# Kernel tuning notes

Hardware: AMD Instinct MI355X
Metric: run time of the kernel (lower is better)

The kernel has to match this reference:

```python
import jax, jax.numpy as jnp
import numpy as np

N_NODES = 100000
N_EDGES = 1600000
N_GRAPHS = 1024
B = 1024
GNN_INP, GNN_HID, GNN_OUT = 64, 128, 64
INP, HID, OUT = 64, 256, 1
EPS = 1e-5  # torch BatchNorm1d default eps


def _bn(h, gamma, beta):
    # training-mode BatchNorm1d: biased batch statistics over dim 0
    m = h.mean(axis=0)
    v = jnp.mean((h - m) ** 2, axis=0)
    return (h - m) * jax.lax.rsqrt(v + EPS) * gamma + beta


def setup_inputs() -> dict:
    key = jax.random.key(0)
    ks = jax.random.split(key, 24)
    s = 0.05
    inp = {
        "x": jax.random.normal(ks[0], (B, INP), jnp.float32),
        "masks": jax.random.randint(ks[1], (B,), 0, N_GRAPHS),
        "gnn_x": jax.random.normal(ks[2], (N_NODES, GNN_INP), jnp.float32),
        "edge_index": jax.random.randint(ks[3], (2, N_EDGES), 0, N_NODES),
        "gnn_batch": jnp.sort(jax.random.randint(ks[4], (N_NODES,), 0, N_GRAPHS)),
        # GCNConv params
        "W_gcn": jax.random.normal(ks[5], (GNN_INP, GNN_HID), jnp.float32) * s,
        "b_gcn": jnp.zeros((GNN_HID,), jnp.float32),
        "g1": jnp.ones((GNN_HID,), jnp.float32), "be1": jnp.zeros((GNN_HID,), jnp.float32),
        "W_lin1": jax.random.normal(ks[6], (GNN_HID, GNN_HID // 2), jnp.float32) * s,
        "b_lin1": jnp.zeros((GNN_HID // 2,), jnp.float32),
        "g2": jnp.ones((GNN_HID // 2,), jnp.float32), "be2": jnp.zeros((GNN_HID // 2,), jnp.float32),
        "W_lin2": jax.random.normal(ks[7], (GNN_HID // 2, GNN_OUT), jnp.float32) * s,
        "b_lin2": jnp.zeros((GNN_OUT,), jnp.float32),
        "g3": jnp.ones((GNN_OUT,), jnp.float32), "be3": jnp.zeros((GNN_OUT,), jnp.float32),
        # head params
        "W_fc1": jax.random.normal(ks[8], (INP + GNN_OUT, HID), jnp.float32) * s,
        "b_fc1": jnp.zeros((HID,), jnp.float32),
        "g4": jnp.ones((HID,), jnp.float32), "be4": jnp.zeros((HID,), jnp.float32),
        "W_fc2": jax.random.normal(ks[9], (HID, HID // 4), jnp.float32) * s,
        "b_fc2": jnp.zeros((HID // 4,), jnp.float32),
        "g5": jnp.ones((HID // 4,), jnp.float32), "be5": jnp.zeros((HID // 4,), jnp.float32),
        "W_fc3": jax.random.normal(ks[10], (HID // 4, OUT), jnp.float32) * s,
        "b_fc3": jnp.zeros((OUT,), jnp.float32),
    }
    return inp


def _forward(x, masks, gnn_x, edge_index, gnn_batch,
             W_gcn, b_gcn, g1, be1, W_lin1, b_lin1, g2, be2, W_lin2, b_lin2,
             g3, be3, W_fc1, b_fc1, g4, be4, W_fc2, b_fc2, g5, be5, W_fc3, b_fc3):
    N = gnn_x.shape[0]
    # --- GCNConv: linear transform, self-loops, sym-normalized scatter-add ---
    h = gnn_x @ W_gcn  # [N, GNN_HID]
    loop = jnp.arange(N)
    src = jnp.concatenate([edge_index[0], loop])
    dst = jnp.concatenate([edge_index[1], loop])
    deg = jax.ops.segment_sum(jnp.ones_like(dst, jnp.float32), dst, num_segments=N)
    dis = jax.lax.rsqrt(deg)  # deg >= 1 thanks to self-loops
    norm = dis[src] * dis[dst]  # [E+N]
    agg = jax.ops.segment_sum(h[src] * norm[:, None], dst, num_segments=N) + b_gcn
    z = jax.nn.relu(_bn(agg, g1, be1))  # dropout = identity (eval)
    # --- global_mean_pool over graph ids ---
    sums = jax.ops.segment_sum(z, gnn_batch, num_segments=N_GRAPHS)
    cnt = jax.ops.segment_sum(jnp.ones((N,), jnp.float32), gnn_batch, num_segments=N_GRAPHS)
    pooled = sums / jnp.maximum(cnt, 1.0)[:, None]  # [G, GNN_HID]
    z = jax.nn.relu(_bn(pooled @ W_lin1 + b_lin1, g2, be2))
    z = _bn(z @ W_lin2 + b_lin2, g3, be3)  # [G, GNN_OUT]
    # --- MixGNN head ---
    g = z[masks]  # [B, GNN_OUT]
    t = jnp.concatenate([x, g], axis=1)
    t = jax.nn.relu(_bn(t @ W_fc1 + b_fc1, g4, be4))
    t = t * t  # Multiply([h, h])
    t = jax.nn.relu(_bn(t @ W_fc2 + b_fc2, g5, be5))
    t = t * t
    t = t * t
    return t @ W_fc3 + b_fc3  # [B, OUT]


def reference(x, masks, gnn_x, edge_index, gnn_batch,
              W_gcn, b_gcn, g1, be1, W_lin1, b_lin1, g2, be2, W_lin2, b_lin2,
              g3, be3, W_fc1, b_fc1, g4, be4, W_fc2, b_fc2, g5, be5, W_fc3, b_fc3):
    return _forward(x, masks, gnn_x, edge_index, gnn_batch,
                    W_gcn, b_gcn, g1, be1, W_lin1, b_lin1, g2, be2, W_lin2, b_lin2,
                    g3, be3, W_fc1, b_fc1, g4, be4, W_fc2, b_fc2, g5, be5, W_fc3, b_fc3)
```

## Files before the change

kernel.cpp:

```cpp
#include <hip/hip_runtime.h>
#include <hip/hip_bf16.h>

#define N_NODES 100000
#define N_EDGES 1600000
#define N_GRAPHS 1024
#define BSZ 1024
#define EPS 1e-5f

#define NBUCK 256
#define BUCKW 391
#define BCAP  8192
#define SRC_MASK 0x1FFFF
#define BIN_CHUNK 4096
#define BIN_BLOCKS 391
#define NCHUNK 512
#define CHUNK_ROWS 196
#define CVT_BLOCKS 6250

#define WS_PSUM    0
#define WS_STATS1  131072
#define WS_STATS2  131200
#define WS_STATS4  131328
#define WS_STATS5  131840
#define WS_M       131968
#define WS_CS      136064
#define WS_ZTOTAL  136128
#define WS_GCUR    136128
#define WS_SCALE1  136384
#define WS_SHIFTP  136512
#define WS_GSTART  136640
#define WS_DIS     137668
#define WS_ROWPTR  237668
#define WS_ROWLEN  337668
#define WS_PACKED  437668
#define WS_CSRC    2534820
#define WS_XH      4631972
#define WS_AGGX    7831972
#define WS_T1      14231972
#define WS_T2      14297508
#define WS_T4      14363044
#define WS_T5      14625188

__device__ inline unsigned short f2bf(float f) {
    unsigned int u = __float_as_uint(f);
    return (unsigned short)((u + 0x7FFFu + ((u >> 16) & 1u)) >> 16);
}

__global__ __launch_bounds__(256) void prep_cvt_kernel(float* __restrict__ ws,
                                                       const int* __restrict__ gbatch,
                                                       const float* __restrict__ x,
                                                       unsigned short* __restrict__ xh) {
    int b = blockIdx.x, tid = threadIdx.x;
    if (b < CVT_BLOCKS) {
        int i = b * 256 + tid;
        float4 f = ((const float4*)x)[i];
        ushort4 h;
        h.x = f2bf(f.x); h.y = f2bf(f.y); h.z = f2bf(f.z); h.w = f2bf(f.w);
        ((ushort4*)xh)[i] = h;
    } else if (b < CVT_BLOCKS + 16) {
        for (int i = (b - CVT_BLOCKS) * 256 + tid; i < WS_ZTOTAL; i += 16 * 256) ws[i] = 0.0f;
    } else if (b == CVT_BLOCKS + 16) {
        ((int*)(ws + WS_GCUR))[tid] = tid * BCAP;
    } else {
        int g = (b - (CVT_BLOCKS + 17)) * 256 + tid;
        int lo = 0, hi = N_NODES;
        while (lo < hi) {
            int mid = (lo + hi) >> 1;
            if (gbatch[mid] < g) lo = mid + 1; else hi = mid;
        }
        int* gstart = (int*)(ws + WS_GSTART);
        gstart[g] = lo;
        if (g == 0) gstart[N_GRAPHS] = N_NODES;
    }
}

__global__ __launch_bounds__(512) void bin_kernel(const int* __restrict__ ei,
                                                  int* __restrict__ gcursor,
                                                  unsigned int* __restrict__ packed) {
    __shared__ unsigned int stage[BIN_CHUNK];
    __shared__ int lh[NBUCK], lbase[NBUCK], lcur[NBUCK], gb[NBUCK];
    const int* src = ei;
    const int* dst = ei + N_EDGES;
    int tid = threadIdx.x;
    int base = blockIdx.x * BIN_CHUNK;
    int n = min(BIN_CHUNK, N_EDGES - base);
    if (tid < NBUCK) lh[tid] = 0;
    __syncthreads();
    for (int i = tid; i < n; i += 512)
        atomicAdd(&lh[dst[base + i] / BUCKW], 1);
    __syncthreads();
    if (tid < NBUCK) lbase[tid] = lh[tid];
    __syncthreads();
    for (int off = 1; off < NBUCK; off <<= 1) {
        int t = (tid < NBUCK && tid >= off) ? lbase[tid - off] : 0;
        __syncthreads();
        if (tid < NBUCK) lbase[tid] += t;
        __syncthreads();
    }
    if (tid < NBUCK) {
        int excl = lbase[tid] - lh[tid];
        lbase[tid] = excl;
        lcur[tid] = excl;
        gb[tid] = atomicAdd(&gcursor[tid], lh[tid]);
    }
    __syncthreads();
    for (int i = tid; i < n; i += 512) {
        int d = dst[base + i];
        int s = src[base + i];
        int bk = d / BUCKW;
        int dl = d - bk * BUCKW;
        int slot = atomicAdd(&lcur[bk], 1);
        stage[slot] = ((unsigned int)dl << 17) | (unsigned int)s;
    }
    __syncthreads();
    int wid = tid >> 6, lane = tid & 63;
    for (int bk = wid; bk < NBUCK; bk += 8) {
        int lo = lbase[bk], go = gb[bk];
        int len = min(lh[bk], (bk + 1) * BCAP - go);
        for (int j = lane; j < len; j += 64)
            packed[go + j] = stage[lo + j];
    }
}

__global__ __launch_bounds__(512) void csr_build_kernel(const unsigned int* __restrict__ packed,
                                                        const int* __restrict__ gcur,
                                                        int* __restrict__ rowptr,
                                                        int* __restrict__ rowlen,
                                                        int* __restrict__ csrc,
                                                        float* __restrict__ dis) {
    __shared__ int dcnt[BUCKW];
    __shared__ int lcur[BUCKW];
    __shared__ int stage[BCAP];
    int b = blockIdx.x, tid = threadIdx.x;
    int e0 = b * BCAP;
    int ecnt = min(gcur[b] - e0, BCAP);
    int nbase = b * BUCKW;
    int nmax = min(BUCKW, N_NODES - nbase);
    for (int i = tid; i < BUCKW; i += 512) dcnt[i] = 0;
    __syncthreads();
    for (int i = tid; i < ecnt; i += 512)
        atomicAdd(&dcnt[packed[e0 + i] >> 17], 1);
    __syncthreads();
    for (int i = tid; i < nmax; i += 512) {
        dis[nbase + i] = rsqrtf((float)dcnt[i] + 1.0f);
        rowlen[nbase + i] = dcnt[i];
    }
    __syncthreads();
    if (tid < 64) {
        int lane = tid;
        int run = 0;
        for (int c = 0; c < BUCKW; c += 64) {
            int idx = c + lane;
            int v = (idx < BUCKW) ? dcnt[idx] : 0;
            int inc = v;
#pragma unroll
            for (int off = 1; off < 64; off <<= 1) {
                int t = __shfl_up(inc, off);
                if (lane >= off) inc += t;
            }
            if (idx < BUCKW) {
                int excl = run + inc - v;
                dcnt[idx] = excl;
                lcur[idx] = excl;
            }
            run += __shfl(inc, 63);
        }
    }
    __syncthreads();
    for (int i = tid; i < nmax; i += 512)
        rowptr[nbase + i] = e0 + dcnt[i];
    for (int i = tid; i < ecnt; i += 512) {
        unsigned int r = packed[e0 + i];
        int slot = atomicAdd(&lcur[r >> 17], 1);
        stage[slot] = (int)(r & SRC_MASK);
    }
    __syncthreads();
    for (int i = tid; i < ecnt; i += 512) csrc[e0 + i] = stage[i];
}

__global__ __launch_bounds__(256) void gather_kernel(const unsigned short* __restrict__ xh,
                                                     const int* __restrict__ rowptr,
                                                     const int* __restrict__ rowlen,
                                                     const int* __restrict__ csrc,
                                                     const float* __restrict__ dis,
                                                     float* __restrict__ aggx) {
    int wid = (blockIdx.x * 256 + threadIdx.x) >> 6;
    int lane = threadIdx.x & 63;
    if (wid >= N_NODES) return;
    int start = rowptr[wid];
    int len = rowlen[wid];
    float dd = dis[wid];
    float self = __uint_as_float((unsigned int)xh[(size_t)wid * 64 + lane] << 16);
    float acc = self * dd * dd;
    for (int j0 = 0; j0 < len; j0 += 64) {
        int cnt = min(64, len - j0);
        int sv = 0;
        float wv = 0.f;
        if (lane < cnt) {
            sv = csrc[start + j0 + lane];
            wv = dis[sv] * dd;
        }
        int iters = (cnt + 7) & ~7;
        for (int k = 0; k < iters; k += 8) {
            int s[8]; float w[8], v[8];
#pragma unroll
            for (int u = 0; u < 8; ++u) {
                s[u] = __shfl(sv, k + u);
                w[u] = __shfl(wv, k + u);
            }
#pragma unroll
            for (int u = 0; u < 8; ++u)
                v[u] = __uint_as_float((unsigned int)xh[(size_t)s[u] * 64 + lane] << 16);
#pragma unroll
            for (int u = 0; u < 8; ++u) acc = fmaf(v[u], w[u], acc);
        }
    }
    aggx[(size_t)wid * 64 + lane] = acc;
}

__global__ __launch_bounds__(256) void moment_kernel(const float* __restrict__ aggx,
                                                     float* __restrict__ M,
                                                     float* __restrict__ CS) {
    __shared__ float rows[8 * 64];
    int c = blockIdx.x, tid = threadIdx.x;
    int r0 = c * CHUNK_ROWS;
    int r1 = min(r0 + CHUNK_ROWS, N_NODES);
    int i0 = (tid >> 6) * 16;
    int j = tid & 63;
    float acc[16] = {};
    float cs = 0.f;
    for (int it = 0; it < (CHUNK_ROWS + 7) / 8; ++it) {
        int sid = tid * 2;
        int grow = r0 + it * 8 + (sid >> 6);
        float2 v = {0.f, 0.f};
        if (grow < r1) v = *(const float2*)(aggx + (size_t)(r0 + it * 8) * 64 + sid);
        __syncthreads();
        *(float2*)(rows + sid) = v;
        __syncthreads();
#pragma unroll
        for (int rr = 0; rr < 8; ++rr) {
            float bj = rows[rr * 64 + j];
            float4 a0 = *(const float4*)(rows + rr * 64 + i0);
            float4 a1 = *(const float4*)(rows + rr * 64 + i0 + 4);
            float4 a2 = *(const float4*)(rows + rr * 64 + i0 + 8);
            float4 a3 = *(const float4*)(rows + rr * 64 + i0 + 12);
            acc[0]  += a0.x * bj; acc[1]  += a0.y * bj; acc[2]  += a0.z * bj; acc[3]  += a0.w * bj;
            acc[4]  += a1.x * bj; acc[5]  += a1.y * bj; acc[6]  += a1.z * bj; acc[7]  += a1.w * bj;
            acc[8]  += a2.x * bj; acc[9]  += a2.y * bj; acc[10] += a2.z * bj; acc[11] += a2.w * bj;
            acc[12] += a3.x * bj; acc[13] += a3.y * bj; acc[14] += a3.z * bj; acc[15] += a3.w * bj;
        }
        if (tid < 64) {
#pragma unroll
            for (int rr = 0; rr < 8; ++rr) cs += rows[rr * 64 + tid];
        }
    }
#pragma unroll
    for (int m = 0; m < 16; ++m)
        unsafeAtomicAdd(&M[(i0 + m) * 64 + j], acc[m]);
    if (tid < 64) unsafeAtomicAdd(&CS[tid], cs);
}

__global__ __launch_bounds__(64) void fold_kernel(const float* __restrict__ M,
                                                  const float* __restrict__ CS,
                                                  const float* __restrict__ W,
                                                  const float* __restrict__ g1,
                                                  const float* __restrict__ be1,
                                                  float* __restrict__ scale1,
                                                  float* __restrict__ shiftp) {
    __shared__ float wcol[64];
    int j = blockIdx.x;
    int lane = threadIdx.x;
    wcol[lane] = W[lane * 128 + j];
    __syncthreads();
    float wl = wcol[lane];
    float t = 0.f;
    const float* Mrow = M + lane * 64;
#pragma unroll 16
    for (int k = 0; k < 64; ++k) t += Mrow[k] * wcol[k];
    float part = t * wl;
    float csp = CS[lane] * wl;
#pragma unroll
    for (int off = 32; off; off >>= 1) {
        part += __shfl_xor(part, off);
        csp  += __shfl_xor(csp, off);
    }
    if (lane == 0) {
        float Ey2 = part * (1.0f / N_NODES);
        float my = csp * (1.0f / N_NODES);
        float var = Ey2 - my * my;
        float sc = g1[j] * rsqrtf(var + EPS);
        scale1[j] = sc;
        shiftp[j] = be1[j] - my * sc;
    }
}

__global__ __launch_bounds__(256) void gemm_pool_kernel(const float* __restrict__ aggx,
                                                        const int* __restrict__ gbatch,
                                                        const float* __restrict__ W,
                                                        const float* __restrict__ scale1,
                                                        const float* __restrict__ shiftp,
                                                        float* __restrict__ psum) {
    __shared__ float Ws[64 * 128];
    __shared__ float As[16 * 64];
    __shared__ float Zs[16 * 128];
    __shared__ int gid[16];
    int tid = threadIdx.x;
    const float4* W4 = (const float4*)W;
    float4* Ws4 = (float4*)Ws;
#pragma unroll
    for (int i = 0; i < 8; ++i) Ws4[tid + i * 256] = W4[tid + i * 256];
    int row0 = blockIdx.x * 16;
    ((float4*)As)[tid] = ((const float4*)(aggx + (size_t)row0 * 64))[tid];
    if (tid < 16) gid[tid] = gbatch[row0 + tid];
    __syncthreads();
    int tx = tid & 31;
    int ty = tid >> 5;
    int r0 = ty * 2;
    float4 sc4 = ((const float4*)scale1)[tx];
    float4 sh4 = ((const float4*)shiftp)[tx];
    float acc[2][4] = {};
#pragma unroll
    for (int k = 0; k < 64; ++k) {
        float a0 = As[r0 * 64 + k];
        float a1 = As[(r0 + 1) * 64 + k];
        float4 w = Ws4[k * 32 + tx];
        acc[0][0] += a0 * w.x; acc[0][1] += a0 * w.y; acc[0][2] += a0 * w.z; acc[0][3] += a0 * w.w;
        acc[1][0] += a1 * w.x; acc[1][1] += a1 * w.y; acc[1][2] += a1 * w.z; acc[1][3] += a1 * w.w;
    }
#pragma unroll
    for (int rr = 0; rr < 2; ++rr) {
        float4 z;
        z.x = fmaxf(acc[rr][0] * sc4.x + sh4.x, 0.f);
        z.y = fmaxf(acc[rr][1] * sc4.y + sh4.y, 0.f);
        z.z = fmaxf(acc[rr][2] * sc4.z + sh4.z, 0.f);
        z.w = fmaxf(acc[rr][3] * sc4.w + sh4.w, 0.f);
        ((float4*)(Zs + (r0 + rr) * 128))[tx] = z;
    }
    __syncthreads();
    if (tid < 128) {
        int c = tid;
        float a = 0.f;
        int g = gid[0];
#pragma unroll
        for (int i = 0; i < 16; ++i) {
            int gi = gid[i];
            if (gi != g) {
                unsafeAtomicAdd(&psum[(size_t)g * 128 + c], a);
                a = 0.f;
                g = gi;
            }
            a += Zs[i * 128 + c];
        }
        unsafeAtomicAdd(&psum[(size_t)g * 128 + c], a);
    }
}

__global__ __launch_bounds__(256) void lin1_kernel(const float* __restrict__ psum,
                                                   const int* __restrict__ gstart,
                                                   const float* __restrict__ W,
                                                   const float* __restrict__ bias,
                                                   float* __restrict__ t1,
                                                   float* __restrict__ stats1) {
    __shared__ float ls[256], ls2[256];
    int tid = threadIdx.x;
    int r = blockIdx.x * 4 + (tid >> 6);
    int c = tid & 63;
    float invc = 1.0f / fmaxf((float)(gstart[r + 1] - gstart[r]), 1.0f);
    float acc = 0.f;
    const float* srow = psum + (size_t)r * 128;
#pragma unroll 8
    for (int k = 0; k < 128; ++k)
        acc += srow[k] * W[k * 64 + c];
    acc = bias[c] + acc * invc;
    t1[r * 64 + c] = acc;
    ls[tid] = acc; ls2[tid] = acc * acc;
    __syncthreads();
    if (tid < 64) {
        float s = ls[tid] + ls[tid + 64] + ls[tid + 128] + ls[tid + 192];
        float q = ls2[tid] + ls2[tid + 64] + ls2[tid + 128] + ls2[tid + 192];
        unsafeAtomicAdd(&stats1[c], s);
        unsafeAtomicAdd(&stats1[64 + c], q);
    }
}

__global__ __launch_bounds__(256) void lin2_kernel(const float* __restrict__ t1,
                                                   const float* __restrict__ stats1,
                                                   const float* __restrict__ g,
                                                   const float* __restrict__ be,
                                                   const float* __restrict__ W,
                                                   const float* __restrict__ bias,
                                                   float* __restrict__ t2,
                                                   float* __restrict__ stats2) {
    __shared__ float sc[64], sh[64];
    __shared__ float ls[256], ls2[256];
    int tid = threadIdx.x;
    if (tid < 64) {
        float m = stats1[tid] * (1.0f / BSZ);
        float var = stats1[64 + tid] * (1.0f / BSZ) - m * m;
        float s = g[tid] * rsqrtf(var + EPS);
        sc[tid] = s; sh[tid] = be[tid] - m * s;
    }
    __syncthreads();
    int r = blockIdx.x * 4 + (tid >> 6);
    int c = tid & 63;
    float acc = bias[c];
    const float* row = t1 + (size_t)r * 64;
#pragma unroll 8
    for (int k = 0; k < 64; ++k) {
        float z = fmaxf(row[k] * sc[k] + sh[k], 0.f);
        acc += z * W[k * 64 + c];
    }
    t2[r * 64 + c] = acc;
    ls[tid] = acc; ls2[tid] = acc * acc;
    __syncthreads();
    if (tid < 64) {
        float s = ls[tid] + ls[tid + 64] + ls[tid + 128] + ls[tid + 192];
        float q = ls2[tid] + ls2[tid + 64] + ls2[tid + 128] + ls2[tid + 192];
        unsafeAtomicAdd(&stats2[c], s);
        unsafeAtomicAdd(&stats2[64 + c], q);
    }
}

__global__ __launch_bounds__(1024) void fc1_kernel(const float* __restrict__ x,
                                                   const int* __restrict__ masks,
                                                   const float* __restrict__ t2,
                                                   const float* __restrict__ stats2,
                                                   const float* __restrict__ g3,
                                                   const float* __restrict__ be3,
                                                   const float* __restrict__ W,
                                                   const float* __restrict__ bias,
                                                   float* __restrict__ t4,
                                                   float* __restrict__ stats4) {
    __shared__ float sc[64], sh[64];
    __shared__ float cat[4][128];
    __shared__ float ls[1024], ls2[1024];
    int tid = threadIdx.x;
    if (tid < 64) {
        float m = stats2[tid] * (1.0f / BSZ);
        float var = stats2[64 + tid] * (1.0f / BSZ) - m * m;
        float s = g3[tid] * rsqrtf(var + EPS);
        sc[tid] = s; sh[tid] = be3[tid] - m * s;
    }
    __syncthreads();
    int r0 = blockIdx.x * 4;
    if (tid < 512) {
        int i = tid >> 7;
        int k = tid & 127;
        int r = r0 + i;
        float v;
        if (k < 64) {
            v = x[r * 64 + k];
        } else {
            int mrow = masks[r];
            int kk = k - 64;
            v = t2[mrow * 64 + kk] * sc[kk] + sh[kk];
        }
        cat[i][k] = v;
    }
    __syncthreads();
    int i = tid >> 8;
    int c = tid & 255;
    float acc = bias[c];
#pragma unroll 8
    for (int k = 0; k < 128; ++k)
        acc += cat[i][k] * W[k * 256 + c];
    t4[(size_t)(r0 + i) * 256 + c] = acc;
    ls[tid] = acc; ls2[tid] = acc * acc;
    __syncthreads();
    if (tid < 256) {
        float s = ls[tid] + ls[tid + 256] + ls[tid + 512] + ls[tid + 768];
        float q = ls2[tid] + ls2[tid + 256] + ls2[tid + 512] + ls2[tid + 768];
        unsafeAtomicAdd(&stats4[c], s);
        unsafeAtomicAdd(&stats4[256 + c], q);
    }
}

__global__ __launch_bounds__(256) void fc2_kernel(const float* __restrict__ t4,
                                                  const float* __restrict__ stats4,
                                                  const float* __restrict__ g4,
                                                  const float* __restrict__ be4,
                                                  const float* __restrict__ W,
                                                  const float* __restrict__ bias,
                                                  float* __restrict__ t5,
                                                  float* __restrict__ stats5) {
    __shared__ float sc[256], sh[256];
    __shared__ float ls[256], ls2[256];
    int tid = threadIdx.x;
    {
        float m = stats4[tid] * (1.0f / BSZ);
        float var = stats4[256 + tid] * (1.0f / BSZ) - m * m;
        float s = g4[tid] * rsqrtf(var + EPS);
        sc[tid] = s; sh[tid] = be4[tid] - m * s;
    }
    __syncthreads();
    int r = blockIdx.x * 4 + (tid >> 6);
    int c = tid & 63;
    float acc = bias[c];
    const float* row = t4 + (size_t)r * 256;
#pragma unroll 8
    for (int k = 0; k < 256; ++k) {
        float z = fmaxf(row[k] * sc[k] + sh[k], 0.f);
        z *= z;
        acc += z * W[k * 64 + c];
    }
    t5[r * 64 + c] = acc;
    ls[tid] = acc; ls2[tid] = acc * acc;
    __syncthreads();
    if (tid < 64) {
        float s = ls[tid] + ls[tid + 64] + ls[tid + 128] + ls[tid + 192];
        float q = ls2[tid] + ls2[tid + 64] + ls2[tid + 128] + ls2[tid + 192];
        unsafeAtomicAdd(&stats5[c], s);
        unsafeAtomicAdd(&stats5[64 + c], q);
    }
}

__global__ __launch_bounds__(256) void fc3_kernel(const float* __restrict__ t5,
                                                  const float* __restrict__ stats5,
                                                  const float* __restrict__ g5,
                                                  const float* __restrict__ be5,
                                                  const float* __restrict__ W,
                                                  const float* __restrict__ bias,
                                                  float* __restrict__ out) {
    __shared__ float sc[64], sh[64];
    int tid = threadIdx.x;
    if (tid < 64) {
        float m = stats5[tid] * (1.0f / BSZ);
        float var = stats5[64 + tid] * (1.0f / BSZ) - m * m;
        float s = g5[tid] * rsqrtf(var + EPS);
        sc[tid] = s; sh[tid] = be5[tid] - m * s;
    }
    __syncthreads();
    int r = blockIdx.x * 256 + tid;
    float acc = bias[0];
    const float* row = t5 + (size_t)r * 64;
#pragma unroll
    for (int k = 0; k < 64; ++k) {
        float z = fmaxf(row[k] * sc[k] + sh[k], 0.f);
        z = z * z;
        z = z * z;
        acc += z * W[k];
    }
    out[r] = acc;
}

extern "C" void kernel_launch(void* const* d_in, const int* in_sizes, int n_in,
                              void* d_out, int out_size, void* d_ws, size_t ws_size,
                              hipStream_t stream) {
    const float* x      = (const float*)d_in[0];
    const int*   masks  = (const int*)d_in[1];
    const float* gnn_x  = (const float*)d_in[2];
    const int*   ei     = (const int*)d_in[3];
    const int*   gbatch = (const int*)d_in[4];
    const float* W_gcn  = (const float*)d_in[5];
    const float* b_gcn  = (const float*)d_in[6];
    const float* g1     = (const float*)d_in[7];
    const float* be1    = (const float*)d_in[8];
    const float* W_lin1 = (const float*)d_in[9];
    const float* b_lin1 = (const float*)d_in[10];
    const float* g2     = (const float*)d_in[11];
    const float* be2    = (const float*)d_in[12];
    const float* W_lin2 = (const float*)d_in[13];
    const float* b_lin2 = (const float*)d_in[14];
    const float* g3     = (const float*)d_in[15];
    const float* be3    = (const float*)d_in[16];
    const float* W_fc1  = (const float*)d_in[17];
    const float* b_fc1  = (const float*)d_in[18];
    const float* g4     = (const float*)d_in[19];
    const float* be4    = (const float*)d_in[20];
    const float* W_fc2  = (const float*)d_in[21];
    const float* b_fc2  = (const float*)d_in[22];
    const float* g5     = (const float*)d_in[23];
    const float* be5    = (const float*)d_in[24];
    const float* W_fc3  = (const float*)d_in[25];
    const float* b_fc3  = (const float*)d_in[26];
    (void)b_gcn;

    float* ws = (float*)d_ws;
    float* psum   = ws + WS_PSUM;
    float* stats1 = ws + WS_STATS1;
    float* stats2 = ws + WS_STATS2;
    float* stats4 = ws + WS_STATS4;
    float* stats5 = ws + WS_STATS5;
    float* Mbuf   = ws + WS_M;
    float* CSbuf  = ws + WS_CS;
    int*   gcur   = (int*)(ws + WS_GCUR);
    float* scale1 = ws + WS_SCALE1;
    float* shiftp = ws + WS_SHIFTP;
    int*   gstart = (int*)(ws + WS_GSTART);
    float* dis    = ws + WS_DIS;
    int*   rowptr = (int*)(ws + WS_ROWPTR);
    int*   rowlen = (int*)(ws + WS_ROWLEN);
    unsigned int* packed = (unsigned int*)(ws + WS_PACKED);
    int*   csrc   = (int*)(ws + WS_CSRC);
    unsigned short* xh = (unsigned short*)(ws + WS_XH);
    float* aggx   = ws + WS_AGGX;
    float* t1     = ws + WS_T1;
    float* t2     = ws + WS_T2;
    float* t4     = ws + WS_T4;
    float* t5     = ws + WS_T5;
    float* out    = (float*)d_out;

    prep_cvt_kernel<<<CVT_BLOCKS + 21, 256, 0, stream>>>(ws, gbatch, gnn_x, xh);
    bin_kernel<<<BIN_BLOCKS, 512, 0, stream>>>(ei, gcur, packed);
    csr_build_kernel<<<NBUCK, 512, 0, stream>>>(packed, gcur, rowptr, rowlen, csrc, dis);
    gather_kernel<<<(N_NODES * 64 + 255) / 256, 256, 0, stream>>>(xh, rowptr, rowlen, csrc, dis, aggx);
    moment_kernel<<<NCHUNK, 256, 0, stream>>>(aggx, Mbuf, CSbuf);
    fold_kernel<<<128, 64, 0, stream>>>(Mbuf, CSbuf, W_gcn, g1, be1, scale1, shiftp);
    gemm_pool_kernel<<<N_NODES / 16, 256, 0, stream>>>(aggx, gbatch, W_gcn, scale1, shiftp, psum);
    lin1_kernel<<<256, 256, 0, stream>>>(psum, gstart, W_lin1, b_lin1, t1, stats1);
    lin2_kernel<<<256, 256, 0, stream>>>(t1, stats1, g2, be2, W_lin2, b_lin2, t2, stats2);
    fc1_kernel<<<256, 1024, 0, stream>>>(x, masks, t2, stats2, g3, be3, W_fc1, b_fc1, t4, stats4);
    fc2_kernel<<<256, 256, 0, stream>>>(t4, stats4, g4, be4, W_fc2, b_fc2, t5, stats5);
    fc3_kernel<<<4, 256, 0, stream>>>(t5, stats5, g5, be5, W_fc3, b_fc3, out);
}
```

Before: 242.5 us.

## Store aggregated features as bf16, cache packed edges in LDS, unroll gather wider

The aggregated node features (aggx) are now written as bf16 instead of fp32, which halves the write traffic in the gather and the read traffic in the moment and gemm_pool kernels. The csr_build kernel keeps the packed edge words in shared memory so the global array is read once instead of twice. The gather inner loop is unrolled to 16 neighbours so more loads are in flight at once. In exchange, the BN statistics and the GEMM input lose precision, and the wider unroll raises register use and adds wasted iterations for low-degree nodes.

```diff
diff --git a/kernel.cpp b/kernel.cpp
--- a/kernel.cpp
+++ b/kernel.cpp
@@ -36,14 +36,17 @@
 #define WS_CSRC    2534820
 #define WS_XH      4631972
 #define WS_AGGX    7831972
-#define WS_T1      14231972
-#define WS_T2      14297508
-#define WS_T4      14363044
-#define WS_T5      14625188
+#define WS_T1      11031972
+#define WS_T2      11097508
+#define WS_T4      11163044
+#define WS_T5      11425188
 
 __device__ inline unsigned short f2bf(float f) {
     unsigned int u = __float_as_uint(f);
     return (unsigned short)((u + 0x7FFFu + ((u >> 16) & 1u)) >> 16);
+}
+__device__ inline float bf2f(unsigned short h) {
+    return __uint_as_float((unsigned int)h << 16);
 }
 
 __global__ __launch_bounds__(256) void prep_cvt_kernel(float* __restrict__ ws,
@@ -128,6 +131,7 @@
                                                         int* __restrict__ rowlen,
                                                         int* __restrict__ csrc,
                                                         float* __restrict__ dis) {
+    __shared__ unsigned int pk[BCAP];
     __shared__ int dcnt[BUCKW];
     __shared__ int lcur[BUCKW];
     __shared__ int stage[BCAP];
@@ -138,8 +142,11 @@
     int nmax = min(BUCKW, N_NODES - nbase);
     for (int i = tid; i < BUCKW; i += 512) dcnt[i] = 0;
     __syncthreads();
-    for (int i = tid; i < ecnt; i += 512)
-        atomicAdd(&dcnt[packed[e0 + i] >> 17], 1);
+    for (int i = tid; i < ecnt; i += 512) {
+        unsigned int r = packed[e0 + i];
+        pk[i] = r;
+        atomicAdd(&dcnt[r >> 17], 1);
+    }
     __syncthreads();
     for (int i = tid; i < nmax; i += 512) {
         dis[nbase + i] = rsqrtf((float)dcnt[i] + 1.0f);
@@ -170,7 +177,7 @@
     for (int i = tid; i < nmax; i += 512)
         rowptr[nbase + i] = e0 + dcnt[i];
     for (int i = tid; i < ecnt; i += 512) {
-        unsigned int r = packed[e0 + i];
+        unsigned int r = pk[i];
         int slot = atomicAdd(&lcur[r >> 17], 1);
         stage[slot] = (int)(r & SRC_MASK);
     }
@@ -183,14 +190,14 @@
                                                      const int* __restrict__ rowlen,
                                                      const int* __restrict__ csrc,
                                                      const float* __restrict__ dis,
-                                                     float* __restrict__ aggx) {
+                                                     unsigned short* __restrict__ aggx) {
     int wid = (blockIdx.x * 256 + threadIdx.x) >> 6;
     int lane = threadIdx.x & 63;
     if (wid >= N_NODES) return;
     int start = rowptr[wid];
     int len = rowlen[wid];
     float dd = dis[wid];
-    float self = __uint_as_float((unsigned int)xh[(size_t)wid * 64 + lane] << 16);
+    float self = bf2f(xh[(size_t)wid * 64 + lane]);
     float acc = self * dd * dd;
     for (int j0 = 0; j0 < len; j0 += 64) {
         int cnt = min(64, len - j0);
@@ -200,25 +207,25 @@
             sv = csrc[start + j0 + lane];
             wv = dis[sv] * dd;
         }
-        int iters = (cnt + 7) & ~7;
-        for (int k = 0; k < iters; k += 8) {
-            int s[8]; float w[8], v[8];
-#pragma unroll
-            for (int u = 0; u < 8; ++u) {
+        int iters = (cnt + 15) & ~15;
+        for (int k = 0; k < iters; k += 16) {
+            int s[16]; float w[16], v[16];
+#pragma unroll
+            for (int u = 0; u < 16; ++u) {
                 s[u] = __shfl(sv, k + u);
                 w[u] = __shfl(wv, k + u);
             }
 #pragma unroll
-            for (int u = 0; u < 8; ++u)
-                v[u] = __uint_as_float((unsigned int)xh[(size_t)s[u] * 64 + lane] << 16);
-#pragma unroll
-            for (int u = 0; u < 8; ++u) acc = fmaf(v[u], w[u], acc);
-        }
-    }
-    aggx[(size_t)wid * 64 + lane] = acc;
-}
-
-__global__ __launch_bounds__(256) void moment_kernel(const float* __restrict__ aggx,
+            for (int u = 0; u < 16; ++u)
+                v[u] = bf2f(xh[(size_t)s[u] * 64 + lane]);
+#pragma unroll
+            for (int u = 0; u < 16; ++u) acc = fmaf(v[u], w[u], acc);
+        }
+    }
+    aggx[(size_t)wid * 64 + lane] = f2bf(acc);
+}
+
+__global__ __launch_bounds__(256) void moment_kernel(const unsigned short* __restrict__ aggx,
                                                      float* __restrict__ M,
                                                      float* __restrict__ CS) {
     __shared__ float rows[8 * 64];
@@ -233,7 +240,10 @@
         int sid = tid * 2;
         int grow = r0 + it * 8 + (sid >> 6);
         float2 v = {0.f, 0.f};
-        if (grow < r1) v = *(const float2*)(aggx + (size_t)(r0 + it * 8) * 64 + sid);
+        if (grow < r1) {
+            ushort2 h = *(const ushort2*)(aggx + (size_t)(r0 + it * 8) * 64 + sid);
+            v.x = bf2f(h.x); v.y = bf2f(h.y);
+        }
         __syncthreads();
         *(float2*)(rows + sid) = v;
         __syncthreads();
@@ -294,7 +304,7 @@
     }
 }
 
-__global__ __launch_bounds__(256) void gemm_pool_kernel(const float* __restrict__ aggx,
+__global__ __launch_bounds__(256) void gemm_pool_kernel(const unsigned short* __restrict__ aggx,
                                                         const int* __restrict__ gbatch,
                                                         const float* __restrict__ W,
                                                         const float* __restrict__ scale1,
@@ -310,7 +320,11 @@
 #pragma unroll
     for (int i = 0; i < 8; ++i) Ws4[tid + i * 256] = W4[tid + i * 256];
     int row0 = blockIdx.x * 16;
-    ((float4*)As)[tid] = ((const float4*)(aggx + (size_t)row0 * 64))[tid];
+    {
+        ushort4 h = ((const ushort4*)(aggx + (size_t)row0 * 64))[tid];
+        float4 f; f.x = bf2f(h.x); f.y = bf2f(h.y); f.z = bf2f(h.z); f.w = bf2f(h.w);
+        ((float4*)As)[tid] = f;
+    }
     if (tid < 16) gid[tid] = gbatch[row0 + tid];
     __syncthreads();
     int tx = tid & 31;
@@ -592,8 +606,8 @@
     int*   rowlen = (int*)(ws + WS_ROWLEN);
     unsigned int* packed = (unsigned int*)(ws + WS_PACKED);
     int*   csrc   = (int*)(ws + WS_CSRC);
-    unsigned short* xh = (unsigned short*)(ws + WS_XH);
-    float* aggx   = ws + WS_AGGX;
+    unsigned short* xh   = (unsigned short*)(ws + WS_XH);
+    unsigned short* aggx = (unsigned short*)(ws + WS_AGGX);
     float* t1     = ws + WS_T1;
     float* t2     = ws + WS_T2;
     float* t4     = ws + WS_T4;
```

Measured after the change: 237.2 us. 2.2% less time.
